# Performance work log

Measured on AMD Instinct MI355X. Metric: run time of the kernel, lower is better.

The kernel has to match this reference:

```python
import jax, jax.numpy as jnp
import numpy as np

N_NODES = 50000
EPS_NORM = 1e-12
EPS_ENT = 1e-8

def _l2norm(x):
    # torch.nn.functional.normalize: x / clamp(||x||, min=1e-12)
    n = jnp.sqrt(jnp.sum(x * x, axis=-1, keepdims=True))
    return x / jnp.maximum(n, EPS_NORM)

def _layer(hidden, src, dst, edge_type, multi_emb, proto_emb):
    # hidden: [N,H]; multi_emb: [R,P,H]; proto_emb: [P,H]
    inp_j = hidden[src]                          # [E,H] gather
    rel_basis = multi_emb[edge_type]             # [E,P,H] gather
    sims = jnp.einsum('eh,ph->ep', _l2norm(inp_j), _l2norm(proto_emb))  # cosine sim [E,P]
    proto_proba = jax.nn.softmax(sims, axis=1)   # [E,P]
    msg = jnp.einsum('ep,eph->eh', proto_proba, rel_basis)              # [E,H]
    ent = -jnp.sum(proto_proba * jnp.log(proto_proba + EPS_ENT), axis=1)  # [E]
    logits = -ent
    # scatter_softmax over destination index
    seg_max = jax.ops.segment_max(logits, dst, num_segments=N_NODES)
    ex = jnp.exp(logits - seg_max[dst])
    denom = jax.ops.segment_sum(ex, dst, num_segments=N_NODES)
    attn = ex / denom[dst]                       # [E]
    out = jax.ops.segment_sum(attn[:, None] * msg, dst, num_segments=N_NODES)  # [N,H]
    return out

def setup_inputs() -> dict:
    key = jax.random.key(0)
    ks = jax.random.split(key, 6)
    E = 800000
    H, R, P, L = 128, 18, 18, 3  # num_layers=4 -> 3 NBFCluttr layers
    edge_index = jax.random.randint(ks[0], (2, E), 0, N_NODES, dtype=jnp.int64) if jax.config.read('jax_enable_x64') else jax.random.randint(ks[0], (2, E), 0, N_NODES, dtype=jnp.int32)
    edge_type = jax.random.randint(ks[1], (E,), 0, R, dtype=edge_index.dtype)
    tail_indices = jax.random.randint(ks[2], (1024,), 0, N_NODES, dtype=edge_index.dtype)
    multi_embeddings = jax.random.uniform(ks[3], (L, R, P, H), dtype=jnp.float32)
    proto_embeddings = jax.random.uniform(ks[4], (L, P, H), dtype=jnp.float32)
    source_embedding = jax.random.uniform(ks[5], (H,), dtype=jnp.float32)
    return {"edge_index": edge_index, "edge_type": edge_type, "tail_indices": tail_indices,
            "multi_embeddings": multi_embeddings, "proto_embeddings": proto_embeddings,
            "source_embedding": source_embedding}

def reference(edge_index, edge_type, tail_indices, multi_embeddings, proto_embeddings, source_embedding):
    src, dst = edge_index[0], edge_index[1]
    H = source_embedding.shape[0]
    # boundary condition: source node gets source_embedding, rest zero
    hidden = jnp.zeros((N_NODES, H), dtype=source_embedding.dtype).at[0].set(source_embedding)
    L = multi_embeddings.shape[0]
    for l in range(L):  # small fixed loop over structurally distinct layers
        hidden = _layer(hidden, src, dst, edge_type, multi_embeddings[l], proto_embeddings[l])
    # apply_classifier, eval_mode=True, use_mlp_classifier=False -> cosine sims to last layer prototypes
    out_emb = hidden[tail_indices]               # [B,H]
    sims = jnp.einsum('nh,ph->np', _l2norm(out_emb), _l2norm(proto_embeddings[-1]))
    return sims  # gumbel_softmax_sample with eval_mode=True returns logits unchanged
```

## Files before the change

kernel.cpp:

```cpp
#include <hip/hip_runtime.h>
#include <hip/hip_bf16.h>


#define N_NODES 50000
#define H 128
#define P 18
#define RP 324
#define KPAD 352
#define K0PAD 64
#define ELLW 64
#define NPART 8
#define NODES_PER_PART 6250

typedef _Float16 half8 __attribute__((ext_vector_type(8)));
typedef float floatx4 __attribute__((ext_vector_type(4)));

__global__ __launch_bounds__(256) void ell_kernel(const int* __restrict__ src,
                                                  const int* __restrict__ dst,
                                                  const int* __restrict__ etype,
                                                  unsigned* __restrict__ cur,
                                                  unsigned* __restrict__ ep, int E) {
  int part = blockIdx.x & (NPART - 1);
  int i = (blockIdx.x >> 3) * 256 + threadIdx.x;
  if (i >= E) return;
  int d = dst[i];
  int lo = part * NODES_PER_PART;
  if (d < lo || d >= lo + NODES_PER_PART) return;
  unsigned pos = atomicAdd(&cur[d], 1u);
  if (pos < ELLW)
    ep[(size_t)d * ELLW + pos] = (unsigned)src[i] | ((unsigned)etype[i] << 20);
}

__global__ __launch_bounds__(64) void protoq0_kernel(const float* __restrict__ proto,
                                                     const float* __restrict__ semb,
                                                     float* __restrict__ pN,
                                                     float* __restrict__ q0r) {
  int row = blockIdx.x, l = threadIdx.x;
  if (row < 54) {
    float a = proto[row * H + l], b = proto[row * H + 64 + l];
    float ss = a * a + b * b;
    for (int m = 32; m > 0; m >>= 1) ss += __shfl_xor(ss, m, 64);
    float inv = 1.f / fmaxf(sqrtf(ss), 1e-12f);
    pN[row * H + l] = a * inv;
    pN[row * H + 64 + l] = b * inv;
    return;
  }
  float s0 = semb[l], s1 = semb[l + 64];
  float ss = s0 * s0 + s1 * s1;
  float dot[P];
#pragma unroll
  for (int p = 0; p < P; p++) {
    float a = proto[p * H + l], b = proto[p * H + 64 + l];
    float rn = a * a + b * b;
    for (int m = 32; m > 0; m >>= 1) rn += __shfl_xor(rn, m, 64);
    float rinv = 1.f / fmaxf(sqrtf(rn), 1e-12f);
    dot[p] = (s0 * a + s1 * b) * rinv;
  }
  for (int m = 1; m <= 32; m <<= 1) {
    ss += __shfl_xor(ss, m, 64);
#pragma unroll
    for (int p = 0; p < P; p++) dot[p] += __shfl_xor(dot[p], m, 64);
  }
  float inv = 1.f / fmaxf(sqrtf(ss), 1e-12f);
  float sum = 0.f;
#pragma unroll
  for (int p = 0; p < P; p++) {
    dot[p] = __expf(dot[p] * inv - 1.f);
    sum += dot[p];
  }
  float isum = 1.f / sum, ent = 0.f;
#pragma unroll
  for (int p = 0; p < P; p++) {
    dot[p] *= isum;
    ent -= dot[p] * __logf(dot[p] + 1e-8f);
  }
  float w = __expf(-ent);
  if (l < P) q0r[l] = w * dot[l];
}

__global__ __launch_bounds__(256) void bprep_kernel(const float* __restrict__ multi,
                                                    const float* __restrict__ q0r,
                                                    _Float16* __restrict__ Btg,
                                                    _Float16* __restrict__ Btl0,
                                                    unsigned* __restrict__ cur) {
  int idx = blockIdx.x * 256 + threadIdx.x;
  if (idx < N_NODES) cur[idx] = 0u;
  if (idx < 2 * H * KPAD) {
    int l = idx / (H * KPAD), rem = idx - l * (H * KPAD);
    int h = rem / KPAD, k = rem - h * KPAD;
    const float* B = multi + (size_t)(l + 1) * RP * H;
    Btg[idx] = (k < RP) ? (_Float16)B[k * H + h] : (_Float16)0.f;
    return;
  }
  int idx2 = idx - 2 * H * KPAD;
  if (idx2 >= H * K0PAD) return;
  int h = idx2 >> 6, k = idx2 & 63;
  float pr = 1.f / 18.f, ent = 0.f;
#pragma unroll
  for (int p = 0; p < P; p++) ent -= pr * __logf(pr + 1e-8f);
  float qc = __expf(-ent) * pr;
  float v = 0.f;
  if (k < P) {
#pragma unroll
    for (int p = 0; p < P; p++) v += qc * multi[(k * P + p) * H + h];
  } else if (k < 2 * P) {
    int r = k - P;
#pragma unroll
    for (int p = 0; p < P; p++) v += (q0r[p] - qc) * multi[(r * P + p) * H + h];
  }
  Btl0[h * K0PAD + k] = (_Float16)v;
}

__global__ __launch_bounds__(256) void hist_kernel(const unsigned* __restrict__ ep,
                                                   const unsigned* __restrict__ cur,
                                                   _Float16* __restrict__ M, int n) {
  int wave = threadIdx.x >> 6, lane = threadIdx.x & 63;
  int nd = blockIdx.x * 4 + wave;
  if (nd >= n) return;
  int cnt = (int)cur[nd];
  if (cnt > ELLW) cnt = ELLW;
  bool a = lane < cnt;
  unsigned pk = a ? ep[(size_t)nd * ELLW + lane] : 0xFFFFFFFFu;
  int r = (int)(pk >> 20);
  unsigned long long zm = __ballot(a && (pk & 0xFFFFFu) == 0u);
  float creg = 0.f, creg0 = 0.f;
#pragma unroll
  for (int rr = 0; rr < P; rr++) {
    unsigned long long m = __ballot(a && (r == rr));
    if (lane == rr) {
      creg = (float)__popcll(m);
      creg0 = (float)__popcll(m & zm);
    }
  }
  int slx = (lane >= P && lane < 2 * P) ? lane - P : 0;
  float v0 = __shfl(creg0, slx, 64);
  float val = (lane < P) ? creg : ((lane < 2 * P) ? v0 : 0.f);
  M[(size_t)nd * K0PAD + lane] = (_Float16)val;
}

__global__ __launch_bounds__(256) void scatter_kernel(const unsigned* __restrict__ ep,
                                                      const unsigned* __restrict__ cur,
                                                      const _Float16* __restrict__ q,
                                                      const int* __restrict__ tl,
                                                      _Float16* __restrict__ M, int n) {
  __shared__ float sl[4][3 * RP];
  int wave = threadIdx.x >> 6, lane = threadIdx.x & 63;
  int t = blockIdx.x * 4 + wave;
  float* s0 = sl[wave];
  for (int i = lane; i < 3 * RP; i += 64) s0[i] = 0.f;
  int sub = lane / 18;
  int j = lane - sub * 18;
  bool act = (sub < 3) && (t < n);
  int cnt = 0;
  size_t b = 0;
  if (t < n) {
    int nd = tl ? tl[t] : t;
    b = (size_t)nd * ELLW;
    cnt = (int)cur[nd];
    if (cnt > ELLW) cnt = ELLW;
  }
  float* ms = s0 + (sub < 3 ? sub : 0) * RP;
  for (int it = 0; it < cnt; it += 9) {
    bool a0 = act && (it + sub < cnt);
    bool a1 = act && (it + 3 + sub < cnt);
    bool a2 = act && (it + 6 + sub < cnt);
    unsigned pk0 = 0, pk1 = 0, pk2 = 0;
    if (a0) pk0 = ep[b + it + sub];
    if (a1) pk1 = ep[b + it + 3 + sub];
    if (a2) pk2 = ep[b + it + 6 + sub];
    float q0 = 0.f, q1 = 0.f, q2 = 0.f;
    if (a0) q0 = (float)q[(size_t)(pk0 & 0xFFFFFu) * P + j];
    if (a1) q1 = (float)q[(size_t)(pk1 & 0xFFFFFu) * P + j];
    if (a2) q2 = (float)q[(size_t)(pk2 & 0xFFFFFu) * P + j];
    if (a0) ms[(pk0 >> 20) * P + j] += q0;
    if (a1) ms[(pk1 >> 20) * P + j] += q1;
    if (a2) ms[(pk2 >> 20) * P + j] += q2;
  }
  if (t < n) {
    for (int k = lane; k < RP; k += 64)
      M[(size_t)t * KPAD + k] = (_Float16)(s0[k] + s0[RP + k] + s0[2 * RP + k]);
    for (int k = RP + lane; k < KPAD; k += 64) M[(size_t)t * KPAD + k] = (_Float16)0.f;
  }
}

template <int MODE>
__global__ __launch_bounds__(256) void gemm_kernel(const _Float16* __restrict__ M,
                                                   const _Float16* __restrict__ Bt,
                                                   const float* __restrict__ pN,
                                                   void* __restrict__ out_ptr, int n,
                                                   int kpad) {
  __shared__ float smem_f[64 * 132];
  _Float16* As = (_Float16*)smem_f;
  _Float16* Bs = (_Float16*)(smem_f + 1024);
  int tid = threadIdx.x;
  int wave = tid >> 6, lane = tid & 63;
  int m15 = lane & 15, quad = lane >> 4;
  int n0 = blockIdx.x * 64;
  floatx4 acc[4][2] = {};

  __shared__ float pns[4 * P * 36];
  for (int i = tid; i < 4 * P * 32; i += 256) {
    int s = i / (P * 32), r = i - s * (P * 32);
    int p = r >> 5, kk = r & 31;
    pns[s * (P * 36) + p * 36 + kk] = pN[p * H + s * 32 + kk];
  }

  for (int kt = 0; kt < (kpad >> 5); kt++) {
    int k0 = kt * 32;
    __syncthreads();
    {
      int row = tid >> 2, kc = (tid & 3) * 8;
      int gr = n0 + row;
      half8 v = {};
      if (gr < n) v = *(const half8*)(M + (size_t)gr * kpad + k0 + kc);
      *(half8*)(As + row * 32 + kc) = v;
    }
    {
      int col = tid >> 1, kc = (tid & 1) * 16;
      const _Float16* srcp = Bt + (size_t)col * kpad + k0 + kc;
      *(half8*)(Bs + col * 32 + kc) = *(const half8*)srcp;
      *(half8*)(Bs + col * 32 + kc + 8) = *(const half8*)(srcp + 8);
    }
    __syncthreads();
    half8 bfrag0 = *(const half8*)(Bs + (wave * 32 + m15) * 32 + quad * 8);
    half8 bfrag1 = *(const half8*)(Bs + (wave * 32 + 16 + m15) * 32 + quad * 8);
#pragma unroll
    for (int mt = 0; mt < 4; mt++) {
      half8 afrag = *(const half8*)(As + (mt * 16 + m15) * 32 + quad * 8);
      acc[mt][0] = __builtin_amdgcn_mfma_f32_16x16x32_f16(afrag, bfrag0, acc[mt][0], 0, 0, 0);
      acc[mt][1] = __builtin_amdgcn_mfma_f32_16x16x32_f16(afrag, bfrag1, acc[mt][1], 0, 0, 0);
    }
  }
  __syncthreads();
#pragma unroll
  for (int mt = 0; mt < 4; mt++)
#pragma unroll
    for (int c = 0; c < 2; c++)
#pragma unroll
      for (int reg = 0; reg < 4; reg++)
        smem_f[(mt * 16 + quad * 4 + reg) * 132 + wave * 32 + c * 16 + m15] = acc[mt][c][reg];
  __syncthreads();
  int node = tid >> 2, sub = tid & 3;
  int gnode = n0 + node;
  const float* trow = smem_f + node * 132 + sub * 32;
  const float* ps = pns + sub * (P * 36);
  float ss = 0.f;
  float dot[P];
#pragma unroll
  for (int p = 0; p < P; p++) dot[p] = 0.f;
#pragma unroll
  for (int k4 = 0; k4 < 8; k4++) {
    float4 y = *(const float4*)(trow + k4 * 4);
    ss += y.x * y.x + y.y * y.y + y.z * y.z + y.w * y.w;
#pragma unroll
    for (int p = 0; p < P; p++) {
      float4 b = *(const float4*)(ps + p * 36 + k4 * 4);
      dot[p] += y.x * b.x + y.y * b.y + y.z * b.z + y.w * b.w;
    }
  }
  for (int m = 1; m <= 2; m <<= 1) {
    ss += __shfl_xor(ss, m, 64);
#pragma unroll
    for (int p = 0; p < P; p++) dot[p] += __shfl_xor(dot[p], m, 64);
  }
  if (gnode < n) {
    float inv = 1.f / fmaxf(sqrtf(ss), 1e-12f);
    if (MODE == 1) {
      float* outp = (float*)out_ptr;
      for (int p = sub; p < P; p += 4) outp[(size_t)gnode * P + p] = dot[p] * inv;
    } else {
      float sum = 0.f;
#pragma unroll
      for (int p = 0; p < P; p++) {
        dot[p] = __expf(dot[p] * inv - 1.f);
        sum += dot[p];
      }
      float isum = 1.f / sum, ent = 0.f;
#pragma unroll
      for (int p = 0; p < P; p++) {
        dot[p] *= isum;
        ent -= dot[p] * __logf(dot[p] + 1e-8f);
      }
      float w = __expf(-ent);
      _Float16* qp = (_Float16*)out_ptr;
      for (int p = sub; p < P; p += 4) qp[(size_t)gnode * P + p] = (_Float16)(w * dot[p]);
    }
  }
}

extern "C" void kernel_launch(void* const* d_in, const int* in_sizes, int n_in,
                              void* d_out, int out_size, void* d_ws, size_t ws_size,
                              hipStream_t stream) {
  const int* eidx = (const int*)d_in[0];
  int E = in_sizes[0] / 2;
  const int* src = eidx;
  const int* dst = eidx + E;
  const int* etype = (const int*)d_in[1];
  const int* tails = (const int*)d_in[2];
  int T = in_sizes[2];
  const float* multi = (const float*)d_in[3];
  const float* proto = (const float*)d_in[4];
  const float* semb = (const float*)d_in[5];
  float* out = (float*)d_out;

  char* w = (char*)d_ws;
  auto alloc = [&](size_t bytes) {
    char* p = w;
    w += (bytes + 255) & ~(size_t)255;
    return p;
  };
  _Float16* q = (_Float16*)alloc((size_t)N_NODES * P * 2);
  float* q0r = (float*)alloc((size_t)P * 4);
  float* pNs = (float*)alloc((size_t)3 * P * H * 4);
  _Float16* Mg = (_Float16*)alloc((size_t)N_NODES * KPAD * 2);
  _Float16* Btg = (_Float16*)alloc((size_t)2 * H * KPAD * 2);
  _Float16* Btl0 = (_Float16*)alloc((size_t)H * K0PAD * 2);
  unsigned* cur = (unsigned*)alloc((size_t)N_NODES * 4);
  unsigned* ep = (unsigned*)alloc((size_t)N_NODES * ELLW * 4);

  int eb = (E + 255) / 256;

  protoq0_kernel<<<55, 64, 0, stream>>>(proto, semb, pNs, q0r);
  bprep_kernel<<<(2 * H * KPAD + H * K0PAD + 255) / 256, 256, 0, stream>>>(multi, q0r, Btg,
                                                                           Btl0, cur);

  ell_kernel<<<eb * NPART, 256, 0, stream>>>(src, dst, etype, cur, ep, E);

  hist_kernel<<<(N_NODES + 3) / 4, 256, 0, stream>>>(ep, cur, Mg, N_NODES);
  gemm_kernel<0><<<(N_NODES + 63) / 64, 256, 0, stream>>>(Mg, Btl0, pNs + (size_t)1 * P * H, q,
                                                          N_NODES, K0PAD);

  scatter_kernel<<<(N_NODES + 3) / 4, 256, 0, stream>>>(ep, cur, q, nullptr, Mg, N_NODES);
  gemm_kernel<0><<<(N_NODES + 63) / 64, 256, 0, stream>>>(Mg, Btg, pNs + (size_t)2 * P * H, q,
                                                          N_NODES, KPAD);

  scatter_kernel<<<(T + 3) / 4, 256, 0, stream>>>(ep, cur, q, tails, Mg, T);
  gemm_kernel<1><<<(T + 63) / 64, 256, 0, stream>>>(Mg, Btg + (size_t)H * KPAD,
                                                    pNs + (size_t)2 * P * H, out, T, KPAD);
}
```

Measured before the change: 237.7 us.

## Build relation histogram with atomics in ELL pass and merge prep kernels

Relation-count histograms are now accumulated with global atomics inside the ELL construction kernel rather than in a separate per-node ballot kernel. The first GEMM reads the u32 histogram directly and converts it to fp16. The prototype normalization, q0 computation and B preparation are merged into one prep kernel that also zeroes the histogram. This cuts launches and one pass over the ELL array, at the cost of extra atomics, a 12.8MB zeroing pass and wider GEMM input reads.

```diff
diff --git a/kernel.cpp b/kernel.cpp
--- a/kernel.cpp
+++ b/kernel.cpp
@@ -11,6 +11,8 @@
 #define ELLW 64
 #define NPART 8
 #define NODES_PER_PART 6250
+#define PREP_MAIN_BLOCKS 3125
+#define HISTW4 800000
 
 typedef _Float16 half8 __attribute__((ext_vector_type(8)));
 typedef float floatx4 __attribute__((ext_vector_type(4)));
@@ -19,24 +21,36 @@
                                                   const int* __restrict__ dst,
                                                   const int* __restrict__ etype,
                                                   unsigned* __restrict__ cur,
-                                                  unsigned* __restrict__ ep, int E) {
+                                                  unsigned* __restrict__ ep,
+                                                  unsigned* __restrict__ hist, int E) {
   int part = blockIdx.x & (NPART - 1);
   int i = (blockIdx.x >> 3) * 256 + threadIdx.x;
   if (i >= E) return;
   int d = dst[i];
   int lo = part * NODES_PER_PART;
   if (d < lo || d >= lo + NODES_PER_PART) return;
+  int s = src[i];
+  int r = etype[i];
   unsigned pos = atomicAdd(&cur[d], 1u);
   if (pos < ELLW)
-    ep[(size_t)d * ELLW + pos] = (unsigned)src[i] | ((unsigned)etype[i] << 20);
-}
-
-__global__ __launch_bounds__(64) void protoq0_kernel(const float* __restrict__ proto,
-                                                     const float* __restrict__ semb,
-                                                     float* __restrict__ pN,
-                                                     float* __restrict__ q0r) {
-  int row = blockIdx.x, l = threadIdx.x;
-  if (row < 54) {
+    ep[(size_t)d * ELLW + pos] = (unsigned)s | ((unsigned)r << 20);
+  atomicAdd(&hist[(size_t)d * K0PAD + r], 1u);
+  if (s == 0) atomicAdd(&hist[(size_t)d * K0PAD + P + r], 1u);
+}
+
+__global__ __launch_bounds__(256) void prep_kernel(const float* __restrict__ multi,
+                                                   const float* __restrict__ proto,
+                                                   const float* __restrict__ semb,
+                                                   float* __restrict__ pN,
+                                                   _Float16* __restrict__ Btg,
+                                                   _Float16* __restrict__ Btl0,
+                                                   unsigned* __restrict__ cur,
+                                                   uint4* __restrict__ hist4) {
+  int bid = blockIdx.x;
+  if (bid >= PREP_MAIN_BLOCKS) {
+    int wave = threadIdx.x >> 6, l = threadIdx.x & 63;
+    int row = (bid - PREP_MAIN_BLOCKS) * 4 + wave;
+    if (row >= 54) return;
     float a = proto[row * H + l], b = proto[row * H + 64 + l];
     float ss = a * a + b * b;
     for (int m = 32; m > 0; m >>= 1) ss += __shfl_xor(ss, m, 64);
@@ -45,46 +59,12 @@
     pN[row * H + 64 + l] = b * inv;
     return;
   }
-  float s0 = semb[l], s1 = semb[l + 64];
-  float ss = s0 * s0 + s1 * s1;
-  float dot[P];
-#pragma unroll
-  for (int p = 0; p < P; p++) {
-    float a = proto[p * H + l], b = proto[p * H + 64 + l];
-    float rn = a * a + b * b;
-    for (int m = 32; m > 0; m >>= 1) rn += __shfl_xor(rn, m, 64);
-    float rinv = 1.f / fmaxf(sqrtf(rn), 1e-12f);
-    dot[p] = (s0 * a + s1 * b) * rinv;
-  }
-  for (int m = 1; m <= 32; m <<= 1) {
-    ss += __shfl_xor(ss, m, 64);
-#pragma unroll
-    for (int p = 0; p < P; p++) dot[p] += __shfl_xor(dot[p], m, 64);
-  }
-  float inv = 1.f / fmaxf(sqrtf(ss), 1e-12f);
-  float sum = 0.f;
-#pragma unroll
-  for (int p = 0; p < P; p++) {
-    dot[p] = __expf(dot[p] * inv - 1.f);
-    sum += dot[p];
-  }
-  float isum = 1.f / sum, ent = 0.f;
-#pragma unroll
-  for (int p = 0; p < P; p++) {
-    dot[p] *= isum;
-    ent -= dot[p] * __logf(dot[p] + 1e-8f);
-  }
-  float w = __expf(-ent);
-  if (l < P) q0r[l] = w * dot[l];
-}
-
-__global__ __launch_bounds__(256) void bprep_kernel(const float* __restrict__ multi,
-                                                    const float* __restrict__ q0r,
-                                                    _Float16* __restrict__ Btg,
-                                                    _Float16* __restrict__ Btl0,
-                                                    unsigned* __restrict__ cur) {
-  int idx = blockIdx.x * 256 + threadIdx.x;
+  int idx = bid * 256 + threadIdx.x;
   if (idx < N_NODES) cur[idx] = 0u;
+  if (idx < HISTW4) {
+    uint4 z = {0u, 0u, 0u, 0u};
+    hist4[idx] = z;
+  }
   if (idx < 2 * H * KPAD) {
     int l = idx / (H * KPAD), rem = idx - l * (H * KPAD);
     int h = rem / KPAD, k = rem - h * KPAD;
@@ -95,10 +75,40 @@
   int idx2 = idx - 2 * H * KPAD;
   if (idx2 >= H * K0PAD) return;
   int h = idx2 >> 6, k = idx2 & 63;
-  float pr = 1.f / 18.f, ent = 0.f;
-#pragma unroll
-  for (int p = 0; p < P; p++) ent -= pr * __logf(pr + 1e-8f);
-  float qc = __expf(-ent) * pr;
+  float s0 = semb[k], s1 = semb[k + 64];
+  float ssq = s0 * s0 + s1 * s1;
+  float dq[P];
+#pragma unroll
+  for (int p = 0; p < P; p++) {
+    float a = proto[p * H + k], b = proto[p * H + 64 + k];
+    float rn = a * a + b * b;
+    for (int m = 32; m > 0; m >>= 1) rn += __shfl_xor(rn, m, 64);
+    float rinv = 1.f / fmaxf(sqrtf(rn), 1e-12f);
+    dq[p] = (s0 * a + s1 * b) * rinv;
+  }
+  for (int m = 1; m <= 32; m <<= 1) {
+    ssq += __shfl_xor(ssq, m, 64);
+#pragma unroll
+    for (int p = 0; p < P; p++) dq[p] += __shfl_xor(dq[p], m, 64);
+  }
+  float inv = 1.f / fmaxf(sqrtf(ssq), 1e-12f);
+  float sum = 0.f;
+#pragma unroll
+  for (int p = 0; p < P; p++) {
+    dq[p] = __expf(dq[p] * inv - 1.f);
+    sum += dq[p];
+  }
+  float isum = 1.f / sum, ent = 0.f;
+#pragma unroll
+  for (int p = 0; p < P; p++) {
+    dq[p] *= isum;
+    ent -= dq[p] * __logf(dq[p] + 1e-8f);
+  }
+  float w = __expf(-ent);
+  float pr = 1.f / 18.f, ent0 = 0.f;
+#pragma unroll
+  for (int p = 0; p < P; p++) ent0 -= pr * __logf(pr + 1e-8f);
+  float qc = __expf(-ent0) * pr;
   float v = 0.f;
   if (k < P) {
 #pragma unroll
@@ -106,36 +116,9 @@
   } else if (k < 2 * P) {
     int r = k - P;
 #pragma unroll
-    for (int p = 0; p < P; p++) v += (q0r[p] - qc) * multi[(r * P + p) * H + h];
+    for (int p = 0; p < P; p++) v += (w * dq[p] - qc) * multi[(r * P + p) * H + h];
   }
   Btl0[h * K0PAD + k] = (_Float16)v;
-}
-
-__global__ __launch_bounds__(256) void hist_kernel(const unsigned* __restrict__ ep,
-                                                   const unsigned* __restrict__ cur,
-                                                   _Float16* __restrict__ M, int n) {
-  int wave = threadIdx.x >> 6, lane = threadIdx.x & 63;
-  int nd = blockIdx.x * 4 + wave;
-  if (nd >= n) return;
-  int cnt = (int)cur[nd];
-  if (cnt > ELLW) cnt = ELLW;
-  bool a = lane < cnt;
-  unsigned pk = a ? ep[(size_t)nd * ELLW + lane] : 0xFFFFFFFFu;
-  int r = (int)(pk >> 20);
-  unsigned long long zm = __ballot(a && (pk & 0xFFFFFu) == 0u);
-  float creg = 0.f, creg0 = 0.f;
-#pragma unroll
-  for (int rr = 0; rr < P; rr++) {
-    unsigned long long m = __ballot(a && (r == rr));
-    if (lane == rr) {
-      creg = (float)__popcll(m);
-      creg0 = (float)__popcll(m & zm);
-    }
-  }
-  int slx = (lane >= P && lane < 2 * P) ? lane - P : 0;
-  float v0 = __shfl(creg0, slx, 64);
-  float val = (lane < P) ? creg : ((lane < 2 * P) ? v0 : 0.f);
-  M[(size_t)nd * K0PAD + lane] = (_Float16)val;
 }
 
 __global__ __launch_bounds__(256) void scatter_kernel(const unsigned* __restrict__ ep,
@@ -183,7 +166,7 @@
   }
 }
 
-template <int MODE>
+template <int MODE, int AU32>
 __global__ __launch_bounds__(256) void gemm_kernel(const _Float16* __restrict__ M,
                                                    const _Float16* __restrict__ Bt,
                                                    const float* __restrict__ pN,
@@ -212,7 +195,19 @@
       int row = tid >> 2, kc = (tid & 3) * 8;
       int gr = n0 + row;
       half8 v = {};
-      if (gr < n) v = *(const half8*)(M + (size_t)gr * kpad + k0 + kc);
+      if (AU32) {
+        if (gr < n) {
+          const unsigned* mp = (const unsigned*)M + (size_t)gr * kpad + k0 + kc;
+          uint4 u0 = *(const uint4*)mp;
+          uint4 u1 = *(const uint4*)(mp + 4);
+          v[0] = (_Float16)(float)u0.x; v[1] = (_Float16)(float)u0.y;
+          v[2] = (_Float16)(float)u0.z; v[3] = (_Float16)(float)u0.w;
+          v[4] = (_Float16)(float)u1.x; v[5] = (_Float16)(float)u1.y;
+          v[6] = (_Float16)(float)u1.z; v[7] = (_Float16)(float)u1.w;
+        }
+      } else {
+        if (gr < n) v = *(const half8*)(M + (size_t)gr * kpad + k0 + kc);
+      }
       *(half8*)(As + row * 32 + kc) = v;
     }
     {
@@ -310,31 +305,29 @@
     return p;
   };
   _Float16* q = (_Float16*)alloc((size_t)N_NODES * P * 2);
-  float* q0r = (float*)alloc((size_t)P * 4);
   float* pNs = (float*)alloc((size_t)3 * P * H * 4);
   _Float16* Mg = (_Float16*)alloc((size_t)N_NODES * KPAD * 2);
   _Float16* Btg = (_Float16*)alloc((size_t)2 * H * KPAD * 2);
   _Float16* Btl0 = (_Float16*)alloc((size_t)H * K0PAD * 2);
   unsigned* cur = (unsigned*)alloc((size_t)N_NODES * 4);
   unsigned* ep = (unsigned*)alloc((size_t)N_NODES * ELLW * 4);
+  unsigned* hist = (unsigned*)alloc((size_t)N_NODES * K0PAD * 4);
 
   int eb = (E + 255) / 256;
 
-  protoq0_kernel<<<55, 64, 0, stream>>>(proto, semb, pNs, q0r);
-  bprep_kernel<<<(2 * H * KPAD + H * K0PAD + 255) / 256, 256, 0, stream>>>(multi, q0r, Btg,
-                                                                           Btl0, cur);
-
-  ell_kernel<<<eb * NPART, 256, 0, stream>>>(src, dst, etype, cur, ep, E);
-
-  hist_kernel<<<(N_NODES + 3) / 4, 256, 0, stream>>>(ep, cur, Mg, N_NODES);
-  gemm_kernel<0><<<(N_NODES + 63) / 64, 256, 0, stream>>>(Mg, Btl0, pNs + (size_t)1 * P * H, q,
-                                                          N_NODES, K0PAD);
+  prep_kernel<<<PREP_MAIN_BLOCKS + 14, 256, 0, stream>>>(multi, proto, semb, pNs, Btg,
+                                                         Btl0, cur, (uint4*)hist);
+
+  ell_kernel<<<eb * NPART, 256, 0, stream>>>(src, dst, etype, cur, ep, hist, E);
+
+  gemm_kernel<0, 1><<<(N_NODES + 63) / 64, 256, 0, stream>>>(
+      (const _Float16*)hist, Btl0, pNs + (size_t)1 * P * H, q, N_NODES, K0PAD);
 
   scatter_kernel<<<(N_NODES + 3) / 4, 256, 0, stream>>>(ep, cur, q, nullptr, Mg, N_NODES);
-  gemm_kernel<0><<<(N_NODES + 63) / 64, 256, 0, stream>>>(Mg, Btg, pNs + (size_t)2 * P * H, q,
-                                                          N_NODES, KPAD);
+  gemm_kernel<0, 0><<<(N_NODES + 63) / 64, 256, 0, stream>>>(Mg, Btg, pNs + (size_t)2 * P * H,
+                                                             q, N_NODES, KPAD);
 
   scatter_kernel<<<(T + 3) / 4, 256, 0, stream>>>(ep, cur, q, tails, Mg, T);
-  gemm_kernel<1><<<(T + 63) / 64, 256, 0, stream>>>(Mg, Btg + (size_t)H * KPAD,
-                                                    pNs + (size_t)2 * P * H, out, T, KPAD);
-}
+  gemm_kernel<1, 0><<<(T + 63) / 64, 256, 0, stream>>>(Mg, Btg + (size_t)H * KPAD,
+                                                       pNs + (size_t)2 * P * H, out, T, KPAD);
+}
```

New measurement: 247.0 us. 1.04x slower.
